# Optimization experiments

Measured on AMD Instinct MI355X. Metric: run time of the kernel, lower is better.

Reference implementation:

```python
import jax, jax.numpy as jnp
import numpy as np

VOCAB = 50257
D = 256
N_UTT = 64
L = 512


def gru_scan(x, W_ih, W_hh, b_ih, b_hh):
    # torch nn.GRU (single layer, batch_first) semantics.
    # x: [B, T, d] -> outputs [B, T, d]
    B, T, d = x.shape
    gx = jnp.einsum('btd,gd->btg', x, W_ih) + b_ih  # [B, T, 3d] input gates precomputed
    gx = jnp.transpose(gx, (1, 0, 2))               # [T, B, 3d] for scan over time

    def step(h, gxt):
        gh = h @ W_hh.T + b_hh                      # [B, 3d]
        xr, xz, xn = jnp.split(gxt, 3, axis=-1)
        hr, hz, hn = jnp.split(gh, 3, axis=-1)
        r = jax.nn.sigmoid(xr + hr)
        z = jax.nn.sigmoid(xz + hz)
        n = jnp.tanh(xn + r * hn)
        h_new = (1.0 - z) * n + z * h
        return h_new, h_new

    h0 = jnp.zeros((B, d), x.dtype)
    _, hs = jax.lax.scan(step, h0, gx)              # hs: [T, B, d]
    return jnp.transpose(hs, (1, 0, 2))


def attn_pool(out, w, b):
    # out: [B, T, d]; Linear(d,1) -> softmax over T -> weighted sum
    logits = out @ w + b                            # [B, T]
    weights = jax.nn.softmax(logits, axis=-1)
    return jnp.einsum('bt,btd->bd', weights, out)   # [B, d]


def setup_inputs() -> dict:
    key = jax.random.key(0)
    ks = jax.random.split(key, 16)
    s = 1.0 / np.sqrt(D)
    u = lambda k, shape: jax.random.uniform(k, shape, jnp.float32, -s, s)
    return {
        'tokens': jax.random.randint(ks[0], (N_UTT, L), 0, VOCAB, dtype=jnp.int32),
        'embed': jax.random.normal(ks[1], (VOCAB, D), jnp.float32),
        'wg_Wih': u(ks[2], (3 * D, D)),
        'wg_Whh': u(ks[3], (3 * D, D)),
        'wg_bih': u(ks[4], (3 * D,)),
        'wg_bhh': u(ks[5], (3 * D,)),
        'ua_w': u(ks[6], (D,)),
        'ua_b': u(ks[7], ()),
        'sg_Wih': u(ks[8], (3 * D, D)),
        'sg_Whh': u(ks[9], (3 * D, D)),
        'sg_bih': u(ks[10], (3 * D,)),
        'sg_bhh': u(ks[11], (3 * D,)),
        'da_w': u(ks[12], (D,)),
        'da_b': u(ks[13], ()),
    }


def reference(tokens, embed, wg_Wih, wg_Whh, wg_bih, wg_bhh, ua_w, ua_b,
              sg_Wih, sg_Whh, sg_bih, sg_bhh, da_w, da_b):
    # Word level: embed each utterance, GRU, attention pooling (batched over utterances)
    emb = embed[tokens]                                   # [N, L, d]
    word_out = gru_scan(emb, wg_Wih, wg_Whh, wg_bih, wg_bhh)
    utt_vecs = attn_pool(word_out, ua_w, ua_b)            # [N, d]
    # Sentence level: pad_sequence of [1,d] vectors -> [N, 1, d] (batch=N, seq=1)
    sent_in = utt_vecs[:, None, :]                        # [N, 1, d]
    sent_out = gru_scan(sent_in, sg_Wih, sg_Whh, sg_bih, sg_bhh)
    dialog_vec = attn_pool(sent_out, da_w, da_b)          # [N, d] (softmax over seq len 1)
    return dialog_vec
```

## Files before the change

kernel.cpp:

```cpp
#include <hip/hip_runtime.h>

typedef _Float16 f16x8 __attribute__((ext_vector_type(8)));
typedef float f32x4 __attribute__((ext_vector_type(4)));

constexpr int D = 256;
constexpr int NUTT = 64;
constexpr int L = 512;
constexpr int G = 768;
constexpr int CHUNK = 128;
constexpr int NCH = L / CHUNK;
constexpr int NBLK = 6;
constexpr int NGEMM = NCH * NUTT * NBLK;

__device__ __forceinline__ void lds_barrier() {
  asm volatile("s_waitcnt lgkmcnt(0)\n\ts_barrier" ::: "memory");
}

__device__ __forceinline__ float fast_rcp(float x) {
  return __builtin_amdgcn_rcpf(x);
}
__device__ __forceinline__ float sigm(float x) {
  return fast_rcp(1.0f + __expf(-x));
}
__device__ __forceinline__ float tanh_f(float x) {
  float ax = fabsf(x);
  float e = __expf(-2.0f * ax);
  float r = (1.0f - e) * fast_rcp(1.0f + e);
  return copysignf(r, x);
}

__global__ __launch_bounds__(256) void pack_wih(
    const float* __restrict__ Wih, _Float16* __restrict__ hi,
    _Float16* __restrict__ lo, int* cnt) {
  if (blockIdx.x == 0) cnt[threadIdx.x << 4] = 0;
  const int d = blockIdx.x * 256 + threadIdx.x;
  const int j = d & 7;
  const int l15 = (d >> 3) & 15;
  const int lk = (d >> 7) & 3;
  const int f = (d >> 9) & 7;
  const int it = d >> 12;
  const int g = 16 * it + l15;
  const int k = 32 * f + 8 * lk + j;
  float v = Wih[g * 256 + k];
  _Float16 h = (_Float16)v;
  hi[d] = h;
  lo[d] = (_Float16)(v - (float)h);
}

__global__ __launch_bounds__(512, 2) void hran_mega(
    const int* __restrict__ tokens, const float* __restrict__ embed,
    const _Float16* __restrict__ whi, const _Float16* __restrict__ wlo,
    const float* __restrict__ bih,
    const float* __restrict__ Whh,
    const float* __restrict__ bhh,
    const float* __restrict__ uaw,
    const float* __restrict__ sWih, const float* __restrict__ sbih,
    const float* __restrict__ sbhh,
    float* __restrict__ gx,
    _Float16* __restrict__ wo16,
    int* cnt,
    float* __restrict__ out) {
  __shared__ __align__(16) _Float16 hbuf[2][D];
  __shared__ float pre[3][D];
  __shared__ float lg[L];
  __shared__ float red[16];
  __shared__ float part[D];
  __shared__ __align__(16) float ut[D];

  const int bx = blockIdx.x;
  const int t = threadIdx.x;
  const int w = t >> 6;
  const int lane = t & 63;
  const int l15 = lane & 15;
  const int lk = lane >> 4;

  if (bx >= NUTT) {
    const int gbx = bx - NUTT;
    const int c = gbx / (NUTT * NBLK);
    const int rem = gbx % (NUTT * NBLK);
    const int u = rem / NBLK;
    const int nb = rem % NBLK;
    const int m0 = u * L + c * CHUNK;
    const int n0 = nb * 128;
    const int it0 = nb * 8;

    const int tok = tokens[m0 + 16 * w + l15];
    const float* arow = embed + (size_t)tok * D;
    const f16x8* Bh = (const f16x8*)whi;
    const f16x8* Bl = (const f16x8*)wlo;
    const int fragbase = lk * 16 + l15;

    f32x4 acc[8] = {};
#pragma unroll
    for (int f = 0; f < 8; ++f) {
      const float* ap = arow + 32 * f + 8 * lk;
      float4 v0 = *(const float4*)(ap);
      float4 v1 = *(const float4*)(ap + 4);
      float av[8] = {v0.x, v0.y, v0.z, v0.w, v1.x, v1.y, v1.z, v1.w};
      f16x8 ahi, alo;
#pragma unroll
      for (int j = 0; j < 8; ++j) {
        _Float16 h = (_Float16)av[j];
        ahi[j] = h;
        alo[j] = (_Float16)(av[j] - (float)h);
      }
#pragma unroll
      for (int i = 0; i < 8; ++i) {
        const int frag = ((it0 + i) * 8 + f) * 64 + fragbase;
        f16x8 bhi = Bh[frag];
        f16x8 blo = Bl[frag];
        acc[i] = __builtin_amdgcn_mfma_f32_16x16x32_f16(ahi, bhi, acc[i], 0, 0, 0);
        acc[i] = __builtin_amdgcn_mfma_f32_16x16x32_f16(alo, bhi, acc[i], 0, 0, 0);
        acc[i] = __builtin_amdgcn_mfma_f32_16x16x32_f16(ahi, blo, acc[i], 0, 0, 0);
      }
    }
#pragma unroll
    for (int i = 0; i < 8; ++i) {
      const int n = n0 + 16 * i + l15;
      const float bb = bih[n];
#pragma unroll
      for (int reg = 0; reg < 4; ++reg) {
        const int m = m0 + 16 * w + 4 * lk + reg;
        gx[(size_t)m * G + n] = acc[i][reg] + bb;
      }
    }
    __syncthreads();
    if (t == 0)
      __hip_atomic_fetch_add(&cnt[((u << 2) + c) << 4], 1,
                             __ATOMIC_RELEASE, __HIP_MEMORY_SCOPE_AGENT);
    return;
  }

  const int b = bx;

  f16x8 Bf[6][8];
#pragma unroll
  for (int i = 0; i < 6; ++i) {
    const float* row = Whh + (size_t)(96 * w + 16 * i + l15) * D + 8 * lk;
#pragma unroll
    for (int f = 0; f < 8; ++f) {
      float4 v0 = *(const float4*)(row + 32 * f);
      float4 v1 = *(const float4*)(row + 32 * f + 4);
      Bf[i][f] = f16x8{(_Float16)v0.x, (_Float16)v0.y,
                       (_Float16)v0.z, (_Float16)v0.w,
                       (_Float16)v1.x, (_Float16)v1.y,
                       (_Float16)v1.z, (_Float16)v1.w};
    }
  }

  float bR = 0.0f, bZ = 0.0f, bN = 0.0f;
  float gr = 0.0f, gz = 0.0f, gn = 0.0f;
  float hprev = 0.0f;
  float* gxb = gx + (size_t)b * L * G;
  _Float16* wob = wo16 + (size_t)b * L * D;
  if (t < 256) {
    bR = bhh[t]; bZ = bhh[D + t]; bN = bhh[2 * D + t];
    hbuf[0][t] = (_Float16)0.0f;
  }
  __syncthreads();

  for (int c = 0; c < NCH; ++c) {
    if (t == 0) {
      while (__hip_atomic_load(&cnt[((b << 2) + c) << 4],
                               __ATOMIC_ACQUIRE,
                               __HIP_MEMORY_SCOPE_AGENT) < NBLK)
        __builtin_amdgcn_s_sleep(8);
    }
    __syncthreads();
    __threadfence();
    if (t < 256) {
      const float* gc = gxb + (size_t)(CHUNK * c) * G;
      gr = gc[t]; gz = gc[D + t]; gn = gc[2 * D + t];
    }

    for (int tsl = 0; tsl < CHUNK; ++tsl) {
      const int ts = CHUNK * c + tsl;
      const int cur = ts & 1;
      const _Float16* hb = hbuf[cur];
      f16x8 A[8];
#pragma unroll
      for (int f = 0; f < 8; ++f)
        A[f] = *(const f16x8*)(hb + 32 * f + 8 * lk);

#pragma unroll
      for (int i = 0; i < 6; ++i) {
        f32x4 acc = {0.0f, 0.0f, 0.0f, 0.0f};
#pragma unroll
        for (int f = 0; f < 8; ++f)
          acc = __builtin_amdgcn_mfma_f32_16x16x32_f16(A[f], Bf[i][f], acc,
                                                       0, 0, 0);
        if (lk == 0) {
          const int n = 96 * w + 16 * i + l15;
          pre[n >> 8][n & 255] = acc[0];
        }
      }
      lds_barrier();

      if (t < 256) {
        float aR = pre[0][t], aZ = pre[1][t], aNp = pre[2][t];
        float r = sigm(gr + aR + bR);
        float z = sigm(gz + aZ + bZ);
        float nn = tanh_f(gn + r * (aNp + bN));
        float hn = fmaf(z, hprev - nn, nn);
        hprev = hn;
        _Float16 hf = (_Float16)hn;
        hbuf[cur ^ 1][t] = hf;
        wob[(size_t)ts * D + t] = hf;
        const int tn = ts + 1;
        if (tn & (CHUNK - 1)) {
          const float* gxn = gxb + (size_t)tn * G;
          gr = gxn[t]; gz = gxn[D + t]; gn = gxn[2 * D + t];
        }
      }
      lds_barrier();
    }
  }

  asm volatile("s_waitcnt vmcnt(0)" ::: "memory");
  __syncthreads();

  {
    const float ua0 = uaw[lane], ua1 = uaw[lane + 64];
    const float ua2 = uaw[lane + 128], ua3 = uaw[lane + 192];
    for (int r = 0; r < 64; ++r) {
      const int tt = 64 * w + r;
      const _Float16* row = wob + (size_t)tt * D;
      float p = (float)row[lane] * ua0 + (float)row[lane + 64] * ua1 +
                (float)row[lane + 128] * ua2 + (float)row[lane + 192] * ua3;
#pragma unroll
      for (int off = 32; off; off >>= 1) p += __shfl_down(p, off);
      if (lane == 0) lg[tt] = p;
    }
  }
  __syncthreads();

  {
    float v = lg[t];
    float m = v;
#pragma unroll
    for (int off = 32; off; off >>= 1) m = fmaxf(m, __shfl_xor(m, off));
    if (lane == 0) red[w] = m;
    __syncthreads();
    m = red[0];
#pragma unroll
    for (int i = 1; i < 8; ++i) m = fmaxf(m, red[i]);
    float e = __expf(v - m);
    float s = e;
#pragma unroll
    for (int off = 32; off; off >>= 1) s += __shfl_xor(s, off);
    if (lane == 0) red[8 + w] = s;
    __syncthreads();
    s = red[8];
#pragma unroll
    for (int i = 9; i < 16; ++i) s += red[i];
    lg[t] = e * (1.0f / s);
  }
  __syncthreads();

  {
    const int d = t & 255, half = t >> 8;
    float acc = 0.0f;
    const _Float16* bbp = wob + (size_t)half * 256 * D;
    const float* lgh = lg + half * 256;
#pragma unroll 4
    for (int k = 0; k < 256; ++k)
      acc = fmaf(lgh[k], (float)bbp[(size_t)k * D + d], acc);
    if (half == 1) part[d] = acc;
    __syncthreads();
    if (half == 0) ut[d] = acc + part[d];
    __syncthreads();
  }

  if (t < 256) {
    const int d = t;
    const float* wr = sWih + (size_t)d * D;
    const float* wz = sWih + (size_t)(D + d) * D;
    const float* wn = sWih + (size_t)(2 * D + d) * D;
    float ar = 0.0f, az = 0.0f, an = 0.0f;
    for (int k = 0; k < D; k += 4) {
      float4 vr = *(const float4*)(wr + k);
      float4 vz = *(const float4*)(wz + k);
      float4 vn = *(const float4*)(wn + k);
      float u0 = ut[k], u1 = ut[k + 1], u2 = ut[k + 2], u3 = ut[k + 3];
      ar += vr.x * u0 + vr.y * u1 + vr.z * u2 + vr.w * u3;
      az += vz.x * u0 + vz.y * u1 + vz.z * u2 + vz.w * u3;
      an += vn.x * u0 + vn.y * u1 + vn.z * u2 + vn.w * u3;
    }
    float r = sigm(ar + sbih[d] + sbhh[d]);
    float z = sigm(az + sbih[D + d] + sbhh[D + d]);
    float n = tanh_f(an + sbih[2 * D + d] + r * sbhh[2 * D + d]);
    out[(size_t)b * D + d] = (1.0f - z) * n;
  }
}

extern "C" void kernel_launch(void* const* d_in, const int* in_sizes, int n_in,
                              void* d_out, int out_size, void* d_ws, size_t ws_size,
                              hipStream_t stream) {
  const int* tokens    = (const int*)d_in[0];
  const float* embed   = (const float*)d_in[1];
  const float* wg_Wih  = (const float*)d_in[2];
  const float* wg_Whh  = (const float*)d_in[3];
  const float* wg_bih  = (const float*)d_in[4];
  const float* wg_bhh  = (const float*)d_in[5];
  const float* ua_w    = (const float*)d_in[6];
  const float* sg_Wih  = (const float*)d_in[8];
  const float* sg_bih  = (const float*)d_in[10];
  const float* sg_bhh  = (const float*)d_in[11];
  float* out = (float*)d_out;

  char* ws = (char*)d_ws;
  const size_t GXB = (size_t)NUTT * L * G * 4;
  float* gx = (float*)ws;
  _Float16* whi = (_Float16*)(ws + GXB);
  _Float16* wlo = whi + (size_t)G * D;
  int* cnt = (int*)(ws + GXB + (size_t)2 * G * D * 2);
  _Float16* wo16 = (_Float16*)(ws + GXB + (size_t)2 * G * D * 2 + 16384);

  pack_wih<<<G, 256, 0, stream>>>(wg_Wih, whi, wlo, cnt);
  hran_mega<<<NUTT + NGEMM, 512, 0, stream>>>(
      tokens, embed, whi, wlo, wg_bih, wg_Whh, wg_bhh, ua_w,
      sg_Wih, sg_bih, sg_bhh, gx, wo16, cnt, out);
}
```

Measured before the change: 776.2 us.

## Use persistent producer blocks with smaller early chunks for GRU input-gate GEMM

Replaces the one-block-per-tile input-projection grid with 192 persistent producer blocks that loop over 64-row jobs in row-block-major order. Recurrence chunks become uneven (64, 64, 128, 128, 128 steps), so the first chunk for each utterance is ready sooner and the sequential scan can start earlier. The counter array is doubled to 8 chunk slots per utterance. The aim is to shorten the startup latency before the recurrence begins and to cut the block-launch count, at the cost of producers running fewer concurrent tiles and each tile now using 64-column wave slices.

```diff
diff --git a/kernel.cpp b/kernel.cpp
--- a/kernel.cpp
+++ b/kernel.cpp
@@ -7,10 +7,9 @@
 constexpr int NUTT = 64;
 constexpr int L = 512;
 constexpr int G = 768;
-constexpr int CHUNK = 128;
-constexpr int NCH = L / CHUNK;
 constexpr int NBLK = 6;
-constexpr int NGEMM = NCH * NUTT * NBLK;
+constexpr int NPROD = 192;
+constexpr int NJOBS = 8 * NUTT * NBLK;
 
 __device__ __forceinline__ void lds_barrier() {
   asm volatile("s_waitcnt lgkmcnt(0)\n\ts_barrier" ::: "memory");
@@ -29,10 +28,15 @@
   return copysignf(r, x);
 }
 
+__device__ __constant__ int c_chunk_of_rb[8] = {0, 1, 2, 2, 3, 3, 4, 4};
+
 __global__ __launch_bounds__(256) void pack_wih(
     const float* __restrict__ Wih, _Float16* __restrict__ hi,
     _Float16* __restrict__ lo, int* cnt) {
-  if (blockIdx.x == 0) cnt[threadIdx.x << 4] = 0;
+  if (blockIdx.x == 0) {
+    cnt[threadIdx.x << 4] = 0;
+    cnt[(threadIdx.x + 256) << 4] = 0;
+  }
   const int d = blockIdx.x * 256 + threadIdx.x;
   const int j = d & 7;
   const int l15 = (d >> 3) & 15;
@@ -75,59 +79,64 @@
   const int lk = lane >> 4;
 
   if (bx >= NUTT) {
-    const int gbx = bx - NUTT;
-    const int c = gbx / (NUTT * NBLK);
-    const int rem = gbx % (NUTT * NBLK);
-    const int u = rem / NBLK;
-    const int nb = rem % NBLK;
-    const int m0 = u * L + c * CHUNK;
-    const int n0 = nb * 128;
-    const int it0 = nb * 8;
-
-    const int tok = tokens[m0 + 16 * w + l15];
-    const float* arow = embed + (size_t)tok * D;
+    const int p = bx - NUTT;
     const f16x8* Bh = (const f16x8*)whi;
     const f16x8* Bl = (const f16x8*)wlo;
     const int fragbase = lk * 16 + l15;
-
-    f32x4 acc[8] = {};
-#pragma unroll
-    for (int f = 0; f < 8; ++f) {
-      const float* ap = arow + 32 * f + 8 * lk;
-      float4 v0 = *(const float4*)(ap);
-      float4 v1 = *(const float4*)(ap + 4);
-      float av[8] = {v0.x, v0.y, v0.z, v0.w, v1.x, v1.y, v1.z, v1.w};
-      f16x8 ahi, alo;
-#pragma unroll
-      for (int j = 0; j < 8; ++j) {
-        _Float16 h = (_Float16)av[j];
-        ahi[j] = h;
-        alo[j] = (_Float16)(av[j] - (float)h);
+    const int wr = w & 3;
+    const int wc = w >> 2;
+
+    for (int J = p; J < NJOBS; J += NPROD) {
+      const int rb = J / (NUTT * NBLK);
+      const int rem = J % (NUTT * NBLK);
+      const int u = rem / NBLK;
+      const int nb = rem % NBLK;
+      const int m0 = u * L + rb * 64;
+      const int n0 = nb * 128 + wc * 64;
+      const int it0 = nb * 8 + wc * 4;
+
+      const int tok = tokens[m0 + 16 * wr + l15];
+      const float* arow = embed + (size_t)tok * D;
+
+      f32x4 acc[4] = {};
+#pragma unroll
+      for (int f = 0; f < 8; ++f) {
+        const float* ap = arow + 32 * f + 8 * lk;
+        float4 v0 = *(const float4*)(ap);
+        float4 v1 = *(const float4*)(ap + 4);
+        float av[8] = {v0.x, v0.y, v0.z, v0.w, v1.x, v1.y, v1.z, v1.w};
+        f16x8 ahi, alo;
+#pragma unroll
+        for (int j = 0; j < 8; ++j) {
+          _Float16 h = (_Float16)av[j];
+          ahi[j] = h;
+          alo[j] = (_Float16)(av[j] - (float)h);
+        }
+#pragma unroll
+        for (int i = 0; i < 4; ++i) {
+          const int frag = ((it0 + i) * 8 + f) * 64 + fragbase;
+          f16x8 bhi = Bh[frag];
+          f16x8 blo = Bl[frag];
+          acc[i] = __builtin_amdgcn_mfma_f32_16x16x32_f16(ahi, bhi, acc[i], 0, 0, 0);
+          acc[i] = __builtin_amdgcn_mfma_f32_16x16x32_f16(alo, bhi, acc[i], 0, 0, 0);
+          acc[i] = __builtin_amdgcn_mfma_f32_16x16x32_f16(ahi, blo, acc[i], 0, 0, 0);
+        }
       }
 #pragma unroll
-      for (int i = 0; i < 8; ++i) {
-        const int frag = ((it0 + i) * 8 + f) * 64 + fragbase;
-        f16x8 bhi = Bh[frag];
-        f16x8 blo = Bl[frag];
-        acc[i] = __builtin_amdgcn_mfma_f32_16x16x32_f16(ahi, bhi, acc[i], 0, 0, 0);
-        acc[i] = __builtin_amdgcn_mfma_f32_16x16x32_f16(alo, bhi, acc[i], 0, 0, 0);
-        acc[i] = __builtin_amdgcn_mfma_f32_16x16x32_f16(ahi, blo, acc[i], 0, 0, 0);
+      for (int i = 0; i < 4; ++i) {
+        const int n = n0 + 16 * i + l15;
+        const float bb = bih[n];
+#pragma unroll
+        for (int reg = 0; reg < 4; ++reg) {
+          const int m = m0 + 16 * wr + 4 * lk + reg;
+          gx[(size_t)m * G + n] = acc[i][reg] + bb;
+        }
       }
-    }
-#pragma unroll
-    for (int i = 0; i < 8; ++i) {
-      const int n = n0 + 16 * i + l15;
-      const float bb = bih[n];
-#pragma unroll
-      for (int reg = 0; reg < 4; ++reg) {
-        const int m = m0 + 16 * w + 4 * lk + reg;
-        gx[(size_t)m * G + n] = acc[i][reg] + bb;
-      }
-    }
-    __syncthreads();
-    if (t == 0)
-      __hip_atomic_fetch_add(&cnt[((u << 2) + c) << 4], 1,
-                             __ATOMIC_RELEASE, __HIP_MEMORY_SCOPE_AGENT);
+      __syncthreads();
+      if (t == 0)
+        __hip_atomic_fetch_add(&cnt[((u << 3) + c_chunk_of_rb[rb]) << 4], 1,
+                               __ATOMIC_RELEASE, __HIP_MEMORY_SCOPE_AGENT);
+    }
     return;
   }
 
@@ -159,22 +168,27 @@
   }
   __syncthreads();
 
-  for (int c = 0; c < NCH; ++c) {
+  const int cstart[5] = {0, 64, 128, 256, 384};
+  const int csize[5]  = {64, 64, 128, 128, 128};
+  const int cneed[5]  = {6, 6, 12, 12, 12};
+
+  for (int c = 0; c < 5; ++c) {
     if (t == 0) {
-      while (__hip_atomic_load(&cnt[((b << 2) + c) << 4],
+      while (__hip_atomic_load(&cnt[((b << 3) + c) << 4],
                                __ATOMIC_ACQUIRE,
-                               __HIP_MEMORY_SCOPE_AGENT) < NBLK)
+                               __HIP_MEMORY_SCOPE_AGENT) < cneed[c])
         __builtin_amdgcn_s_sleep(8);
     }
     __syncthreads();
     __threadfence();
     if (t < 256) {
-      const float* gc = gxb + (size_t)(CHUNK * c) * G;
+      const float* gc = gxb + (size_t)cstart[c] * G;
       gr = gc[t]; gz = gc[D + t]; gn = gc[2 * D + t];
     }
 
-    for (int tsl = 0; tsl < CHUNK; ++tsl) {
-      const int ts = CHUNK * c + tsl;
+    const int cs = csize[c];
+    for (int tsl = 0; tsl < cs; ++tsl) {
+      const int ts = cstart[c] + tsl;
       const int cur = ts & 1;
       const _Float16* hb = hbuf[cur];
       f16x8 A[8];
@@ -206,9 +220,8 @@
         _Float16 hf = (_Float16)hn;
         hbuf[cur ^ 1][t] = hf;
         wob[(size_t)ts * D + t] = hf;
-        const int tn = ts + 1;
-        if (tn & (CHUNK - 1)) {
-          const float* gxn = gxb + (size_t)tn * G;
+        if (tsl + 1 < cs) {
+          const float* gxn = gxb + (size_t)(ts + 1) * G;
           gr = gxn[t]; gz = gxn[D + t]; gn = gxn[2 * D + t];
         }
       }
@@ -314,10 +327,10 @@
   _Float16* whi = (_Float16*)(ws + GXB);
   _Float16* wlo = whi + (size_t)G * D;
   int* cnt = (int*)(ws + GXB + (size_t)2 * G * D * 2);
-  _Float16* wo16 = (_Float16*)(ws + GXB + (size_t)2 * G * D * 2 + 16384);
+  _Float16* wo16 = (_Float16*)(ws + GXB + (size_t)2 * G * D * 2 + 32768);
 
   pack_wih<<<G, 256, 0, stream>>>(wg_Wih, whi, wlo, cnt);
-  hran_mega<<<NUTT + NGEMM, 512, 0, stream>>>(
+  hran_mega<<<NUTT + NPROD, 512, 0, stream>>>(
       tokens, embed, whi, wlo, wg_bih, wg_Whh, wg_bhh, ua_w,
       sg_Wih, sg_bih, sg_bhh, gx, wo16, cnt, out);
 }
```

New measurement: 853.0 us. 9.9% more time.
